# Optimization experiments

Hardware: AMD Instinct MI355X
Metric: run time of the kernel (lower is better)

## Reference

```python
import jax, jax.numpy as jnp
import numpy as np

B, S, D = 2, 2048, 1024
H = 16
HD = D // H  # 64
SCALE = 1.0 / np.sqrt(HD)


def setup_inputs() -> dict:
    key = jax.random.key(0)
    k1, k2, k3, k4, k5 = jax.random.split(key, 5)
    std = 0.02
    return {
        "Q_input": jax.random.normal(k1, (B, S, D), dtype=jnp.float32),
        "Wq": jax.random.normal(k2, (D, H * HD), dtype=jnp.float32) * std,
        "Wk": jax.random.normal(k3, (D, HD), dtype=jnp.float32) * std,
        "Wv": jax.random.normal(k4, (D, HD), dtype=jnp.float32) * std,
        "Wo": jax.random.normal(k5, (H * HD, D), dtype=jnp.float32) * std,
    }


def reference(Q_input, Wq, Wk, Wv, Wo):
    b, s, _ = Q_input.shape
    # projections; K/V use a single shared head (MQA)
    Q = (Q_input @ Wq).reshape(b, s, H, HD)   # [b,s,H,hd]
    K = Q_input @ Wk                           # [b,s,hd]
    V = Q_input @ Wv                           # [b,s,hd]
    # scores: broadcast the single KV head across all H query heads
    scores = jnp.einsum("bqhd,bkd->bhqk", Q, K) * SCALE  # [b,H,s,s]
    probs = jax.nn.softmax(scores, axis=-1)
    ctx = jnp.einsum("bhqk,bkd->bqhd", probs, V)          # [b,s,H,hd]
    out = ctx.reshape(b, s, H * HD) @ Wo                  # [b,s,D]
    return out
```

## Files before the change

### kernel.cpp

```cpp
#include <hip/hip_runtime.h>

typedef __attribute__((ext_vector_type(8))) short bf16x8;
typedef __attribute__((ext_vector_type(4))) float f32x4;
typedef __attribute__((ext_vector_type(4))) unsigned int u32x4;
typedef unsigned short u16;

#define MFMA16(a,b,c) __builtin_amdgcn_mfma_f32_16x16x32_bf16((a),(b),(c),0,0,0)

__device__ __forceinline__ u16 f2bf(float f){
  unsigned int u = __float_as_uint(f);
  u += 0x7fffu + ((u >> 16) & 1u);
  return (u16)(u >> 16);
}
__device__ __forceinline__ float bf2f(u16 v){
  return __uint_as_float(((unsigned int)v) << 16);
}
__device__ __forceinline__ unsigned int cvtpk(float lo, float hi){
  unsigned int r;
  asm("v_cvt_pk_bf16_f32 %0, %1, %2" : "=v"(r) : "v"(lo), "v"(hi));
  return r;
}
__device__ __forceinline__ void gload16(const void* g, void* l){
  __builtin_amdgcn_global_load_lds(
      (__attribute__((address_space(1))) void*)g,
      (__attribute__((address_space(3))) void*)l, 16, 0, 0);
}

__global__ __launch_bounds__(256) void mqa_cvt(const float* __restrict__ in,
                                               u16* __restrict__ out, int n8){
  int i = blockIdx.x * 256 + threadIdx.x;
  if (i >= n8) return;
  const float4* p = (const float4*)in;
  float4 a = p[2*i], b = p[2*i+1];
  u16 o[8] = { f2bf(a.x), f2bf(a.y), f2bf(a.z), f2bf(a.w),
               f2bf(b.x), f2bf(b.y), f2bf(b.z), f2bf(b.w) };
  *(bf16x8*)&out[(size_t)i*8] = *(bf16x8*)o;
}

__global__ __launch_bounds__(256) void mqa_tcvt4(
    const float* __restrict__ Wq, const float* __restrict__ Wk,
    const float* __restrict__ Wv, const float* __restrict__ Wo,
    u16* __restrict__ WT, u16* __restrict__ WoT)
{
  __shared__ float t[32][33];
  int bx = blockIdx.x;
  const float* src; u16* dst; int C, cb, rb;
  if (bx < 1024)      { src = Wq; dst = WT;                      C = 1024; int q = bx;        cb = q & 31; rb = q >> 5; }
  else if (bx < 1088) { src = Wk; dst = WT + (size_t)1024*1024;  C = 64;   int q = bx - 1024; cb = q & 1;  rb = q >> 1; }
  else if (bx < 1152) { src = Wv; dst = WT + (size_t)1088*1024;  C = 64;   int q = bx - 1088; cb = q & 1;  rb = q >> 1; }
  else                { src = Wo; dst = WoT;                     C = 1024; int q = bx - 1152; cb = q & 31; rb = q >> 5; }
  int c0 = cb * 32, r0 = rb * 32;
  int x = threadIdx.x & 31, y0 = threadIdx.x >> 5;
  #pragma unroll
  for (int yy = y0; yy < 32; yy += 8)
    t[yy][x] = src[(size_t)(r0 + yy) * C + c0 + x];
  __syncthreads();
  #pragma unroll
  for (int yy = y0; yy < 32; yy += 8)
    dst[(size_t)(c0 + yy) * 1024 + r0 + x] = f2bf(t[x][yy]);
}

template<int EPI>
__global__ __launch_bounds__(256, 4) void mqa_gemm(
    const u16* __restrict__ A, const u16* __restrict__ Bt,
    float* __restrict__ outF, u16* __restrict__ Qb, u16* __restrict__ Kb,
    u16* __restrict__ Vtb, int M, int N, int K, int NT)
{
  __shared__ __align__(16) u16 lds_a[64*32];
  __shared__ __align__(16) u16 lds_b[128*32];
  int bx = blockIdx.x;
  int mt = bx / NT, nt = bx % NT;
  int m0 = mt * 64, n0 = nt * 128;
  int tid = threadIdx.x;
  int wid = tid >> 6, lane = tid & 63;
  int wr = (wid >> 1) * 32, wc = (wid & 1) * 64;
  int lrow = lane >> 2;
  int lk   = (lane & 3) * 8;
  int fr = lane & 15, g8 = (lane >> 4) * 8, fg = lane >> 4;

  f32x4 acc[2][4];
  #pragma unroll
  for (int i = 0; i < 2; ++i)
    #pragma unroll
    for (int j = 0; j < 4; ++j) acc[i][j] = (f32x4)0.f;

  for (int k0 = 0; k0 < K; k0 += 32) {
    #pragma unroll
    for (int cc = 0; cc < 3; ++cc) {
      int c = 3*wid + cc;
      if (c < 4) gload16(&A [(size_t)(m0 + c*16 + lrow) * K + k0 + lk], &lds_a[c*512]);
      else       gload16(&Bt[(size_t)(n0 + (c-4)*16 + lrow) * K + k0 + lk], &lds_b[(c-4)*512]);
    }
    __syncthreads();
    bf16x8 af[2], bfr[4];
    #pragma unroll
    for (int i = 0; i < 2; ++i) af[i] = *(const bf16x8*)&lds_a[(wr + i*16 + fr)*32 + g8];
    #pragma unroll
    for (int j = 0; j < 4; ++j) bfr[j] = *(const bf16x8*)&lds_b[(wc + j*16 + fr)*32 + g8];
    #pragma unroll
    for (int i = 0; i < 2; ++i)
      #pragma unroll
      for (int j = 0; j < 4; ++j)
        acc[i][j] = MFMA16(af[i], bfr[j], acc[i][j]);
    __syncthreads();
  }

  #pragma unroll
  for (int i = 0; i < 2; ++i) {
    #pragma unroll
    for (int j = 0; j < 4; ++j) {
      int ncol = n0 + wc + j*16 + fr;
      #pragma unroll
      for (int r = 0; r < 4; ++r) {
        int m = m0 + wr + i*16 + fg*4 + r;
        float v = acc[i][j][r];
        if (EPI == 0) {
          outF[(size_t)m * N + ncol] = v;
        } else {
          u16 bv = f2bf(v);
          if (ncol < 1024) {
            Qb[(size_t)m * 1024 + ncol] = bv;
          } else if (ncol < 1088) {
            Kb[(size_t)m * 64 + (ncol - 1024)] = bv;
          } else {
            int b = m >> 11, s = m & 2047;
            int k = s & 63;
            int pos = (k & 35) | ((k & 12) << 1) | ((k & 16) >> 2);
            Vtb[((size_t)b * 64 + (ncol - 1088)) * 2048 + (s & ~63) + pos] = bv;
          }
        }
      }
    }
  }
}

__global__ __launch_bounds__(256, 3) void mqa_attn(
    const u16* __restrict__ Qb, const u16* __restrict__ Kb,
    const u16* __restrict__ Vtb, u16* __restrict__ Opart,
    float* __restrict__ Lpart)
{
  const float C1 = 0.18033688011112042f;
  const float MC = 32.f * C1;
  int qt = blockIdx.x, h = blockIdx.y;
  int b = blockIdx.z >> 1, sp = blockIdx.z & 1;
  int part = blockIdx.z;
  int tid = threadIdx.x, wid = tid >> 6, lane = tid & 63;
  int fr = lane & 15, g = lane >> 4;
  int q0 = qt * 128 + wid * 32;

  __shared__ __align__(16) u16 KT[2][64*64];
  __shared__ __align__(16) u16 VT[2][64*64];

  const u16* Qbase = Qb + (size_t)b * 2048 * 1024 + (size_t)h * 64;
  const u16* Kbase = Kb + (size_t)b * 2048 * 64;
  const u16* Vbase = Vtb + (size_t)b * 64 * 2048;

  int srow = lane >> 3;
  int scol = ((lane & 7) ^ srow) * 8;

  bf16x8 qfv[2][2];
  #pragma unroll
  for (int qf_ = 0; qf_ < 2; ++qf_)
    #pragma unroll
    for (int ks = 0; ks < 2; ++ks)
      qfv[qf_][ks] = *(const bf16x8*)&Qbase[(size_t)(q0 + qf_*16 + fr) * 1024 + ks*32 + g*8];

  f32x4 oacc[2][4];
  #pragma unroll
  for (int qf_ = 0; qf_ < 2; ++qf_)
    #pragma unroll
    for (int vf = 0; vf < 4; ++vf) oacc[qf_][vf] = (f32x4)0.f;
  float lacc0 = 0.f, lacc1 = 0.f;

  const int kb0 = sp * 16;

  #pragma unroll
  for (int j = 0; j < 2; ++j) {
    int row = wid*16 + j*8 + srow;
    gload16(&Kbase[(size_t)(kb0*64 + row) * 64 + scol], &KT[0][(wid*16 + j*8) * 64]);
    gload16(&Vbase[(size_t)row * 2048 + kb0*64 + scol], &VT[0][(wid*16 + j*8) * 64]);
  }
  __syncthreads();

  int cur = 0;
  for (int kb = kb0; kb < kb0 + 16; ++kb) {
    int ntl = (kb + 1 < kb0 + 16) ? kb + 1 : kb0;
    #pragma unroll
    for (int j = 0; j < 2; ++j) {
      int row = wid*16 + j*8 + srow;
      gload16(&Kbase[(size_t)(ntl*64 + row) * 64 + scol], &KT[cur^1][(wid*16 + j*8) * 64]);
      gload16(&Vbase[(size_t)row * 2048 + ntl*64 + scol], &VT[cur^1][(wid*16 + j*8) * 64]);
    }

    const u16* kc = &KT[cur][0];
    const u16* vc = &VT[cur][0];

    f32x4 sacc[2][4];
    #pragma unroll
    for (int qf_ = 0; qf_ < 2; ++qf_)
      #pragma unroll
      for (int kf = 0; kf < 4; ++kf) sacc[qf_][kf] = (f32x4)0.f;

    __builtin_amdgcn_s_setprio(1);
    #pragma unroll
    for (int ks = 0; ks < 2; ++ks) {
      #pragma unroll
      for (int kf = 0; kf < 4; ++kf) {
        bf16x8 kfr = *(const bf16x8*)&kc[(kf*16 + fr)*64 + (((ks*4+g) ^ (fr&7)))*8];
        sacc[0][kf] = MFMA16(kfr, qfv[0][ks], sacc[0][kf]);
        sacc[1][kf] = MFMA16(kfr, qfv[1][ks], sacc[1][kf]);
      }
    }
    __builtin_amdgcn_s_setprio(0);

    unsigned int pk0[8], pk1[8];
    float s0 = 0.f, s1 = 0.f;
    #pragma unroll
    for (int kf = 0; kf < 4; ++kf) {
      float a0 = __builtin_amdgcn_exp2f(sacc[0][kf][0] * C1 - MC);
      float a1 = __builtin_amdgcn_exp2f(sacc[0][kf][1] * C1 - MC);
      float a2 = __builtin_amdgcn_exp2f(sacc[0][kf][2] * C1 - MC);
      float a3 = __builtin_amdgcn_exp2f(sacc[0][kf][3] * C1 - MC);
      s0 += (a0 + a1) + (a2 + a3);
      pk0[2*kf]   = cvtpk(a0, a1);
      pk0[2*kf+1] = cvtpk(a2, a3);
      float b0 = __builtin_amdgcn_exp2f(sacc[1][kf][0] * C1 - MC);
      float b1 = __builtin_amdgcn_exp2f(sacc[1][kf][1] * C1 - MC);
      float b2 = __builtin_amdgcn_exp2f(sacc[1][kf][2] * C1 - MC);
      float b3 = __builtin_amdgcn_exp2f(sacc[1][kf][3] * C1 - MC);
      s1 += (b0 + b1) + (b2 + b3);
      pk1[2*kf]   = cvtpk(b0, b1);
      pk1[2*kf+1] = cvtpk(b2, b3);
    }
    lacc0 += s0;
    lacc1 += s1;

    __builtin_amdgcn_s_setprio(1);
    #pragma unroll
    for (int ks2 = 0; ks2 < 2; ++ks2) {
      u32x4 w0 = { pk0[4*ks2], pk0[4*ks2+1], pk0[4*ks2+2], pk0[4*ks2+3] };
      u32x4 w1 = { pk1[4*ks2], pk1[4*ks2+1], pk1[4*ks2+2], pk1[4*ks2+3] };
      bf16x8 pA0 = __builtin_bit_cast(bf16x8, w0);
      bf16x8 pA1 = __builtin_bit_cast(bf16x8, w1);
      #pragma unroll
      for (int vf = 0; vf < 4; ++vf) {
        bf16x8 vfr = *(const bf16x8*)&vc[(vf*16 + fr)*64 + (((ks2*4+g) ^ (fr&7)))*8];
        oacc[0][vf] = MFMA16(pA0, vfr, oacc[0][vf]);
        oacc[1][vf] = MFMA16(pA1, vfr, oacc[1][vf]);
      }
    }
    __builtin_amdgcn_s_setprio(0);

    __syncthreads();
    cur ^= 1;
  }

  lacc0 += __shfl_xor(lacc0, 16); lacc0 += __shfl_xor(lacc0, 32);
  lacc1 += __shfl_xor(lacc1, 16); lacc1 += __shfl_xor(lacc1, 32);

  #pragma unroll
  for (int qf_ = 0; qf_ < 2; ++qf_) {
    #pragma unroll
    for (int r = 0; r < 4; ++r) {
      int row = q0 + qf_*16 + g*4 + r;
      #pragma unroll
      for (int vf = 0; vf < 4; ++vf) {
        int col = h*64 + vf*16 + fr;
        Opart[((size_t)part * 2048 + row) * 1024 + col] = f2bf(oacc[qf_][vf][r]);
      }
    }
  }
  if (g == 0) {
    int q = q0 + fr;
    size_t base = ((size_t)part * 16 + h) * 2048;
    Lpart[base + q]      = lacc0;
    Lpart[base + q + 16] = lacc1;
  }
}

__global__ __launch_bounds__(256) void mqa_merge(
    const u16* __restrict__ Opart, const float* __restrict__ Lpart,
    u16* __restrict__ Ctx)
{
  int idx = blockIdx.x * 256 + threadIdx.x;
  int cg  = idx & 255;
  int row = (idx >> 8) & 2047;
  int b   = idx >> 19;
  int h   = cg >> 4;
  size_t mb0 = ((size_t)(b*2 + 0) * 16 + h) * 2048 + row;
  size_t mb1 = ((size_t)(b*2 + 1) * 16 + h) * 2048 + row;
  float rl = 1.f / (Lpart[mb0] + Lpart[mb1]);
  size_t o0 = ((size_t)(b*2 + 0) * 2048 + row) * 1024 + cg * 4;
  size_t o1 = ((size_t)(b*2 + 1) * 2048 + row) * 1024 + cg * 4;
  ushort4 a = *(const ushort4*)&Opart[o0];
  ushort4 c = *(const ushort4*)&Opart[o1];
  u16 o[4];
  o[0] = f2bf((bf2f(a.x) + bf2f(c.x)) * rl);
  o[1] = f2bf((bf2f(a.y) + bf2f(c.y)) * rl);
  o[2] = f2bf((bf2f(a.z) + bf2f(c.z)) * rl);
  o[3] = f2bf((bf2f(a.w) + bf2f(c.w)) * rl);
  *(ushort4*)&Ctx[((size_t)b * 2048 + row) * 1024 + cg * 4] = *(ushort4*)o;
}

extern "C" void kernel_launch(void* const* d_in, const int* in_sizes, int n_in,
                              void* d_out, int out_size, void* d_ws, size_t ws_size,
                              hipStream_t stream)
{
  const float* Qin = (const float*)d_in[0];
  const float* Wq  = (const float*)d_in[1];
  const float* Wk  = (const float*)d_in[2];
  const float* Wv  = (const float*)d_in[3];
  const float* Wo  = (const float*)d_in[4];
  float* out = (float*)d_out;

  u16* Xb  = (u16*)d_ws;
  u16* WT  = Xb  + (size_t)4096*1024;
  u16* WoT = WT  + (size_t)1152*1024;
  u16* Qb  = WoT + (size_t)1024*1024;
  u16* Kb  = Qb  + (size_t)4096*1024;
  u16* Vtb = Kb  + (size_t)4096*64;
  u16* Ctx = Vtb + (size_t)2*64*2048;
  float* Lpart = (float*)(Ctx + (size_t)4096*1024);

  u16* Opart = (u16*)d_out;

  mqa_cvt<<<2048, 256, 0, stream>>>(Qin, Xb, 4096*1024/8);
  mqa_tcvt4<<<2176, 256, 0, stream>>>(Wq, Wk, Wv, Wo, WT, WoT);

  mqa_gemm<1><<<64*9, 256, 0, stream>>>(Xb, WT, nullptr, Qb, Kb, Vtb,
                                        4096, 1152, 1024, 9);
  mqa_attn<<<dim3(16,16,4), 256, 0, stream>>>(Qb, Kb, Vtb, Opart, Lpart);
  mqa_merge<<<4096, 256, 0, stream>>>(Opart, Lpart, Ctx);
  mqa_gemm<0><<<64*8, 256, 0, stream>>>(Ctx, WoT, out, nullptr, nullptr, nullptr,
                                        4096, 1024, 1024, 8);
}
```

Before: 114.2 us.

## Double-buffer GEMM LDS tiles and widen attention query tile per wave

The GEMM now keeps two LDS buffers and issues the next k-slice's global-to-LDS loads before computing on the current one, dropping one barrier per iteration so load latency can overlap MFMA work. The attention kernel gives each wave 64 query rows instead of 32, halving the grid and reusing each K/V tile and V fragment across four query fragments, with V fragments hoisted into registers. This roughly doubles accumulator register use, so launch bounds drop to 2 blocks per SIMD, trading occupancy and parallelism (512 blocks) for fewer LDS loads per MFMA.

```diff
diff --git a/kernel.cpp b/kernel.cpp
--- a/kernel.cpp
+++ b/kernel.cpp
@@ -66,8 +66,8 @@
     float* __restrict__ outF, u16* __restrict__ Qb, u16* __restrict__ Kb,
     u16* __restrict__ Vtb, int M, int N, int K, int NT)
 {
-  __shared__ __align__(16) u16 lds_a[64*32];
-  __shared__ __align__(16) u16 lds_b[128*32];
+  __shared__ __align__(16) u16 lds_a[2][64*32];
+  __shared__ __align__(16) u16 lds_b[2][128*32];
   int bx = blockIdx.x;
   int mt = bx / NT, nt = bx % NT;
   int m0 = mt * 64, n0 = nt * 128;
@@ -84,25 +84,32 @@
     #pragma unroll
     for (int j = 0; j < 4; ++j) acc[i][j] = (f32x4)0.f;
 
-  for (int k0 = 0; k0 < K; k0 += 32) {
+  auto stage = [&](int bi, int k0){
     #pragma unroll
     for (int cc = 0; cc < 3; ++cc) {
       int c = 3*wid + cc;
-      if (c < 4) gload16(&A [(size_t)(m0 + c*16 + lrow) * K + k0 + lk], &lds_a[c*512]);
-      else       gload16(&Bt[(size_t)(n0 + (c-4)*16 + lrow) * K + k0 + lk], &lds_b[(c-4)*512]);
-    }
-    __syncthreads();
+      if (c < 4) gload16(&A [(size_t)(m0 + c*16 + lrow) * K + k0 + lk], &lds_a[bi][c*512]);
+      else       gload16(&Bt[(size_t)(n0 + (c-4)*16 + lrow) * K + k0 + lk], &lds_b[bi][(c-4)*512]);
+    }
+  };
+
+  stage(0, 0);
+  __syncthreads();
+  int cur = 0;
+  for (int k0 = 0; k0 < K; k0 += 32) {
+    if (k0 + 32 < K) stage(cur ^ 1, k0 + 32);
     bf16x8 af[2], bfr[4];
     #pragma unroll
-    for (int i = 0; i < 2; ++i) af[i] = *(const bf16x8*)&lds_a[(wr + i*16 + fr)*32 + g8];
-    #pragma unroll
-    for (int j = 0; j < 4; ++j) bfr[j] = *(const bf16x8*)&lds_b[(wc + j*16 + fr)*32 + g8];
+    for (int i = 0; i < 2; ++i) af[i] = *(const bf16x8*)&lds_a[cur][(wr + i*16 + fr)*32 + g8];
+    #pragma unroll
+    for (int j = 0; j < 4; ++j) bfr[j] = *(const bf16x8*)&lds_b[cur][(wc + j*16 + fr)*32 + g8];
     #pragma unroll
     for (int i = 0; i < 2; ++i)
       #pragma unroll
       for (int j = 0; j < 4; ++j)
         acc[i][j] = MFMA16(af[i], bfr[j], acc[i][j]);
     __syncthreads();
+    cur ^= 1;
   }
 
   #pragma unroll
@@ -134,7 +141,7 @@
   }
 }
 
-__global__ __launch_bounds__(256, 3) void mqa_attn(
+__global__ __launch_bounds__(256, 2) void mqa_attn(
     const u16* __restrict__ Qb, const u16* __restrict__ Kb,
     const u16* __restrict__ Vtb, u16* __restrict__ Opart,
     float* __restrict__ Lpart)
@@ -146,7 +153,7 @@
   int part = blockIdx.z;
   int tid = threadIdx.x, wid = tid >> 6, lane = tid & 63;
   int fr = lane & 15, g = lane >> 4;
-  int q0 = qt * 128 + wid * 32;
+  int q0 = qt * 256 + wid * 64;
 
   __shared__ __align__(16) u16 KT[2][64*64];
   __shared__ __align__(16) u16 VT[2][64*64];
@@ -158,19 +165,19 @@
   int srow = lane >> 3;
   int scol = ((lane & 7) ^ srow) * 8;
 
-  bf16x8 qfv[2][2];
-  #pragma unroll
-  for (int qf_ = 0; qf_ < 2; ++qf_)
+  bf16x8 qfv[4][2];
+  #pragma unroll
+  for (int qf_ = 0; qf_ < 4; ++qf_)
     #pragma unroll
     for (int ks = 0; ks < 2; ++ks)
       qfv[qf_][ks] = *(const bf16x8*)&Qbase[(size_t)(q0 + qf_*16 + fr) * 1024 + ks*32 + g*8];
 
-  f32x4 oacc[2][4];
-  #pragma unroll
-  for (int qf_ = 0; qf_ < 2; ++qf_)
+  f32x4 oacc[4][4];
+  #pragma unroll
+  for (int qf_ = 0; qf_ < 4; ++qf_)
     #pragma unroll
     for (int vf = 0; vf < 4; ++vf) oacc[qf_][vf] = (f32x4)0.f;
-  float lacc0 = 0.f, lacc1 = 0.f;
+  float lacc[4] = {0.f, 0.f, 0.f, 0.f};
 
   const int kb0 = sp * 16;
 
@@ -195,9 +202,9 @@
     const u16* kc = &KT[cur][0];
     const u16* vc = &VT[cur][0];
 
-    f32x4 sacc[2][4];
-    #pragma unroll
-    for (int qf_ = 0; qf_ < 2; ++qf_)
+    f32x4 sacc[4][4];
+    #pragma unroll
+    for (int qf_ = 0; qf_ < 4; ++qf_)
       #pragma unroll
       for (int kf = 0; kf < 4; ++kf) sacc[qf_][kf] = (f32x4)0.f;
 
@@ -207,59 +214,60 @@
       #pragma unroll
       for (int kf = 0; kf < 4; ++kf) {
         bf16x8 kfr = *(const bf16x8*)&kc[(kf*16 + fr)*64 + (((ks*4+g) ^ (fr&7)))*8];
-        sacc[0][kf] = MFMA16(kfr, qfv[0][ks], sacc[0][kf]);
-        sacc[1][kf] = MFMA16(kfr, qfv[1][ks], sacc[1][kf]);
+        #pragma unroll
+        for (int qf_ = 0; qf_ < 4; ++qf_)
+          sacc[qf_][kf] = MFMA16(kfr, qfv[qf_][ks], sacc[qf_][kf]);
       }
     }
     __builtin_amdgcn_s_setprio(0);
 
-    unsigned int pk0[8], pk1[8];
-    float s0 = 0.f, s1 = 0.f;
-    #pragma unroll
-    for (int kf = 0; kf < 4; ++kf) {
-      float a0 = __builtin_amdgcn_exp2f(sacc[0][kf][0] * C1 - MC);
-      float a1 = __builtin_amdgcn_exp2f(sacc[0][kf][1] * C1 - MC);
-      float a2 = __builtin_amdgcn_exp2f(sacc[0][kf][2] * C1 - MC);
-      float a3 = __builtin_amdgcn_exp2f(sacc[0][kf][3] * C1 - MC);
-      s0 += (a0 + a1) + (a2 + a3);
-      pk0[2*kf]   = cvtpk(a0, a1);
-      pk0[2*kf+1] = cvtpk(a2, a3);
-      float b0 = __builtin_amdgcn_exp2f(sacc[1][kf][0] * C1 - MC);
-      float b1 = __builtin_amdgcn_exp2f(sacc[1][kf][1] * C1 - MC);
-      float b2 = __builtin_amdgcn_exp2f(sacc[1][kf][2] * C1 - MC);
-      float b3 = __builtin_amdgcn_exp2f(sacc[1][kf][3] * C1 - MC);
-      s1 += (b0 + b1) + (b2 + b3);
-      pk1[2*kf]   = cvtpk(b0, b1);
-      pk1[2*kf+1] = cvtpk(b2, b3);
-    }
-    lacc0 += s0;
-    lacc1 += s1;
-
-    __builtin_amdgcn_s_setprio(1);
-    #pragma unroll
-    for (int ks2 = 0; ks2 < 2; ++ks2) {
-      u32x4 w0 = { pk0[4*ks2], pk0[4*ks2+1], pk0[4*ks2+2], pk0[4*ks2+3] };
-      u32x4 w1 = { pk1[4*ks2], pk1[4*ks2+1], pk1[4*ks2+2], pk1[4*ks2+3] };
-      bf16x8 pA0 = __builtin_bit_cast(bf16x8, w0);
-      bf16x8 pA1 = __builtin_bit_cast(bf16x8, w1);
-      #pragma unroll
-      for (int vf = 0; vf < 4; ++vf) {
-        bf16x8 vfr = *(const bf16x8*)&vc[(vf*16 + fr)*64 + (((ks2*4+g) ^ (fr&7)))*8];
-        oacc[0][vf] = MFMA16(pA0, vfr, oacc[0][vf]);
-        oacc[1][vf] = MFMA16(pA1, vfr, oacc[1][vf]);
-      }
-    }
-    __builtin_amdgcn_s_setprio(0);
+    bf16x8 vfr[8];
+    #pragma unroll
+    for (int i = 0; i < 8; ++i) {
+      int ks2 = i >> 2, vf = i & 3;
+      vfr[i] = *(const bf16x8*)&vc[(vf*16 + fr)*64 + (((ks2*4+g) ^ (fr&7)))*8];
+    }
+
+    #pragma unroll
+    for (int qf_ = 0; qf_ < 4; ++qf_) {
+      unsigned int pk[8];
+      float s0 = 0.f;
+      #pragma unroll
+      for (int kf = 0; kf < 4; ++kf) {
+        float a0 = __builtin_amdgcn_exp2f(sacc[qf_][kf][0] * C1 - MC);
+        float a1 = __builtin_amdgcn_exp2f(sacc[qf_][kf][1] * C1 - MC);
+        float a2 = __builtin_amdgcn_exp2f(sacc[qf_][kf][2] * C1 - MC);
+        float a3 = __builtin_amdgcn_exp2f(sacc[qf_][kf][3] * C1 - MC);
+        s0 += (a0 + a1) + (a2 + a3);
+        pk[2*kf]   = cvtpk(a0, a1);
+        pk[2*kf+1] = cvtpk(a2, a3);
+      }
+      lacc[qf_] += s0;
+
+      __builtin_amdgcn_s_setprio(1);
+      #pragma unroll
+      for (int ks2 = 0; ks2 < 2; ++ks2) {
+        u32x4 w = { pk[4*ks2], pk[4*ks2+1], pk[4*ks2+2], pk[4*ks2+3] };
+        bf16x8 pA = __builtin_bit_cast(bf16x8, w);
+        #pragma unroll
+        for (int vf = 0; vf < 4; ++vf)
+          oacc[qf_][vf] = MFMA16(pA, vfr[ks2*4+vf], oacc[qf_][vf]);
+      }
+      __builtin_amdgcn_s_setprio(0);
+    }
 
     __syncthreads();
     cur ^= 1;
   }
 
-  lacc0 += __shfl_xor(lacc0, 16); lacc0 += __shfl_xor(lacc0, 32);
-  lacc1 += __shfl_xor(lacc1, 16); lacc1 += __shfl_xor(lacc1, 32);
-
-  #pragma unroll
-  for (int qf_ = 0; qf_ < 2; ++qf_) {
+  #pragma unroll
+  for (int qf_ = 0; qf_ < 4; ++qf_) {
+    lacc[qf_] += __shfl_xor(lacc[qf_], 16);
+    lacc[qf_] += __shfl_xor(lacc[qf_], 32);
+  }
+
+  #pragma unroll
+  for (int qf_ = 0; qf_ < 4; ++qf_) {
     #pragma unroll
     for (int r = 0; r < 4; ++r) {
       int row = q0 + qf_*16 + g*4 + r;
@@ -271,10 +279,10 @@
     }
   }
   if (g == 0) {
-    int q = q0 + fr;
     size_t base = ((size_t)part * 16 + h) * 2048;
-    Lpart[base + q]      = lacc0;
-    Lpart[base + q + 16] = lacc1;
+    #pragma unroll
+    for (int qf_ = 0; qf_ < 4; ++qf_)
+      Lpart[base + q0 + qf_*16 + fr] = lacc[qf_];
   }
 }
 
@@ -329,7 +337,7 @@
 
   mqa_gemm<1><<<64*9, 256, 0, stream>>>(Xb, WT, nullptr, Qb, Kb, Vtb,
                                         4096, 1152, 1024, 9);
-  mqa_attn<<<dim3(16,16,4), 256, 0, stream>>>(Qb, Kb, Vtb, Opart, Lpart);
+  mqa_attn<<<dim3(8,16,4), 256, 0, stream>>>(Qb, Kb, Vtb, Opart, Lpart);
   mqa_merge<<<4096, 256, 0, stream>>>(Opart, Lpart, Ctx);
   mqa_gemm<0><<<64*8, 256, 0, stream>>>(Ctx, WoT, out, nullptr, nullptr, nullptr,
                                         4096, 1024, 1024, 8);
```

Measured after the change: 114.6 us. Within noise of the previous version (+0.3%).

## Double-buffer GEMM LDS tiles with K-step 64 and XOR swizzle

Applied to the files above, without the earlier changes.

The projection GEMM now uses two LDS buffers with a K-step of 64. The next tile's global-to-LDS loads are issued before the current tile's MFMAs, and one barrier per iteration replaces two. LDS rows are XOR-swizzled to avoid bank conflicts on the wider 64-element rows. Launch bounds are adjusted (GEMM 4→3 waves, attention 3→4) to fit the larger LDS footprint and trade register budget. A possible gap: the prefetch into the other buffer is only completed by the end-of-loop barrier, and whether the async global_load_lds writes are properly waited for depends on the barrier's implicit vmcnt handling.

```diff
diff --git a/kernel.cpp b/kernel.cpp
--- a/kernel.cpp
+++ b/kernel.cpp
@@ -61,22 +61,23 @@
 }
 
 template<int EPI>
-__global__ __launch_bounds__(256, 4) void mqa_gemm(
+__global__ __launch_bounds__(256, 3) void mqa_gemm(
     const u16* __restrict__ A, const u16* __restrict__ Bt,
     float* __restrict__ outF, u16* __restrict__ Qb, u16* __restrict__ Kb,
     u16* __restrict__ Vtb, int M, int N, int K, int NT)
 {
-  __shared__ __align__(16) u16 lds_a[64*32];
-  __shared__ __align__(16) u16 lds_b[128*32];
+  __shared__ __align__(16) u16 lds_a[2][64*64];
+  __shared__ __align__(16) u16 lds_b[2][128*64];
   int bx = blockIdx.x;
   int mt = bx / NT, nt = bx % NT;
   int m0 = mt * 64, n0 = nt * 128;
   int tid = threadIdx.x;
   int wid = tid >> 6, lane = tid & 63;
   int wr = (wid >> 1) * 32, wc = (wid & 1) * 64;
-  int lrow = lane >> 2;
-  int lk   = (lane & 3) * 8;
-  int fr = lane & 15, g8 = (lane >> 4) * 8, fg = lane >> 4;
+  int srow = lane >> 3;
+  int scol = ((lane & 7) ^ srow) * 8;
+  int fr = lane & 15, g = lane >> 4, fg = lane >> 4;
+  int sw = fr & 7;
 
   f32x4 acc[2][4];
   #pragma unroll
@@ -84,25 +85,45 @@
     #pragma unroll
     for (int j = 0; j < 4; ++j) acc[i][j] = (f32x4)0.f;
 
-  for (int k0 = 0; k0 < K; k0 += 32) {
+  auto stage = [&](int bi, int k0){
     #pragma unroll
     for (int cc = 0; cc < 3; ++cc) {
       int c = 3*wid + cc;
-      if (c < 4) gload16(&A [(size_t)(m0 + c*16 + lrow) * K + k0 + lk], &lds_a[c*512]);
-      else       gload16(&Bt[(size_t)(n0 + (c-4)*16 + lrow) * K + k0 + lk], &lds_b[(c-4)*512]);
+      #pragma unroll
+      for (int j = 0; j < 2; ++j) {
+        if (c < 4) {
+          int row = c*16 + j*8;
+          gload16(&A [(size_t)(m0 + row + srow) * K + k0 + scol], &lds_a[bi][row*64]);
+        } else {
+          int row = (c-4)*16 + j*8;
+          gload16(&Bt[(size_t)(n0 + row + srow) * K + k0 + scol], &lds_b[bi][row*64]);
+        }
+      }
+    }
+  };
+
+  stage(0, 0);
+  __syncthreads();
+  int cur = 0;
+  for (int k0 = 0; k0 < K; k0 += 64) {
+    if (k0 + 64 < K) stage(cur ^ 1, k0 + 64);
+    #pragma unroll
+    for (int ks = 0; ks < 2; ++ks) {
+      bf16x8 af[2], bfr[4];
+      #pragma unroll
+      for (int i = 0; i < 2; ++i)
+        af[i] = *(const bf16x8*)&lds_a[cur][(wr + i*16 + fr)*64 + (((ks*4+g) ^ sw))*8];
+      #pragma unroll
+      for (int j = 0; j < 4; ++j)
+        bfr[j] = *(const bf16x8*)&lds_b[cur][(wc + j*16 + fr)*64 + (((ks*4+g) ^ sw))*8];
+      #pragma unroll
+      for (int i = 0; i < 2; ++i)
+        #pragma unroll
+        for (int j = 0; j < 4; ++j)
+          acc[i][j] = MFMA16(af[i], bfr[j], acc[i][j]);
     }
     __syncthreads();
-    bf16x8 af[2], bfr[4];
-    #pragma unroll
-    for (int i = 0; i < 2; ++i) af[i] = *(const bf16x8*)&lds_a[(wr + i*16 + fr)*32 + g8];
-    #pragma unroll
-    for (int j = 0; j < 4; ++j) bfr[j] = *(const bf16x8*)&lds_b[(wc + j*16 + fr)*32 + g8];
-    #pragma unroll
-    for (int i = 0; i < 2; ++i)
-      #pragma unroll
-      for (int j = 0; j < 4; ++j)
-        acc[i][j] = MFMA16(af[i], bfr[j], acc[i][j]);
-    __syncthreads();
+    cur ^= 1;
   }
 
   #pragma unroll
@@ -134,7 +155,7 @@
   }
 }
 
-__global__ __launch_bounds__(256, 3) void mqa_attn(
+__global__ __launch_bounds__(256, 4) void mqa_attn(
     const u16* __restrict__ Qb, const u16* __restrict__ Kb,
     const u16* __restrict__ Vtb, u16* __restrict__ Opart,
     float* __restrict__ Lpart)
```

After: 101.7 us. 1.12x faster.
